# Optimization experiments

Hardware: AMD Instinct MI355X
Metric: run time of the kernel (lower is better)

The kernel has to match this reference:

```python
import jax, jax.numpy as jnp
import numpy as np

THRESH = 0.3
EPS = 1e-8
M = 256
D = 768


def setup_inputs() -> dict:
    key = jax.random.key(0)
    kx, kb, ka, kn = jax.random.split(key, 4)
    x = jax.random.normal(kx, (1, D), dtype=jnp.float32)
    base = jax.random.normal(kb, (M, D), dtype=jnp.float32)
    # correlate memories with x so that a realistic fraction passes the 0.3 cosine threshold
    alpha = jax.random.uniform(ka, (M,), minval=0.0, maxval=0.8)
    mem = alpha[:, None] * x[0][None, :] + jnp.sqrt(1.0 - alpha**2)[:, None] * base
    # pre-sampled injection noise (original: torch.randn * 0.1 per W element)
    noise = 0.1 * jax.random.normal(kn, (M, M, D), dtype=jnp.float32)
    return {"x": x, "mem": mem, "noise": noise}


def reference(x, mem, noise):
    # x: [1, D] query embedding; mem: [M, D] memory bank (k == memory embeddings)
    d = x.shape[-1]
    xv = x[0]                                   # [D]
    nx = jnp.maximum(jnp.linalg.norm(xv), EPS)
    nm = jnp.linalg.norm(mem, axis=-1)          # [M]
    nm_s = jnp.maximum(nm, EPS)
    Sx = xv.sum()
    Sm = mem.sum(-1)                            # [M]

    kx_dot = mem @ xv                           # [M] dot(k_i, x)
    mx_cos = kx_dot / (nm_s * nx)               # [M] cos(x, m_j) == cos(k_i, x)
    mask = (mx_cos > THRESH).astype(x.dtype)    # active memories A
    cnt = mask.sum()

    km_dot = mem @ mem.T                        # [M, M] dot(k_i, m_j)
    km_cos = km_dot / (nm_s[:, None] * nm_s[None, :])

    # c[a, i] = cos(k_i, m_a) + cos(k_i, x)  (scalar added to all D dims of k_i)
    c = km_cos.T + mx_cos[None, :]              # [M, M]

    # ||k'_{a,i}||^2 = ||k_i||^2 + 2 c sum(k_i) + D c^2
    nkp = jnp.sqrt(jnp.maximum(nm[None, :]**2 + 2.0 * c * Sm[None, :] + d * c**2, EPS**2))

    # cos(k'_{a,i}, x) = (dot(k_i,x) + c*sum(x)) / (||k'|| * ||x||)
    cos_kp_x = (kx_dot[None, :] + c * Sx) / (nkp * nx)

    # mean over a' in A of cos(k'_{a,i}, m_{a'}) in closed form
    A1 = (km_dot * (mask / nm_s)[None, :]).sum(-1)   # [M] (i-indexed)
    A2 = ((mask * Sm) / nm_s).sum()                  # scalar
    denom = nkp * jnp.maximum(cnt, 1.0)
    mean_cos_km = jnp.where(cnt > 0, (A1[None, :] + c * A2) / denom, 0.0)

    # W_{a,i} = k'_{a,i} + mean sim to x + mean sim to active mems; then noise; O_prev = 0
    W = mem[None, :, :] + (c + cos_kp_x + mean_cos_km)[:, :, None]   # [M, M, D]
    out = (W + noise) * mask[:, None, None]     # zero rows for inactive memories
    return out
```

## Files before the change

### kernel.cpp

```cpp
#include <hip/hip_runtime.h>
#include <hip/hip_bf16.h>
#include <math.h>

#define M 256
#define D 768
#define D4 (D/4)
#define THRESH 0.3
#define EPS 1e-8

typedef float vfloat4 __attribute__((ext_vector_type(4)));

#define WS_SM    0
#define WS_NM2   256
#define WS_KX    512
#define WS_MASK  768
#define WS_SX    1024
#define WS_NX2   1025
#define WS_MEMT  2048
#define WS_ST    (2048 + D * M)

__global__ __launch_bounds__(256) void k1_stats_transpose(const float* __restrict__ x,
                                                          const float* __restrict__ mem,
                                                          float* __restrict__ ws) {
    const int r = blockIdx.x;
    const int t = threadIdx.x;
    const float* row = (r < M) ? (mem + (size_t)r * D) : x;

    double s = 0.0, sq = 0.0, dt = 0.0;
    for (int d = t; d < D; d += 256) {
        float mf = row[d];
        double m = (double)mf;
        double xv = (double)x[d];
        s += m; sq += m * m; dt += m * xv;
        if (r < M) ws[WS_MEMT + (d >> 2) * (M * 4) + r * 4 + (d & 3)] = mf;
    }
    __shared__ double sh0[256], sh1[256], sh2[256];
    sh0[t] = s; sh1[t] = sq; sh2[t] = dt;
    __syncthreads();
    for (int k = 128; k > 0; k >>= 1) {
        if (t < k) { sh0[t] += sh0[t + k]; sh1[t] += sh1[t + k]; sh2[t] += sh2[t + k]; }
        __syncthreads();
    }
    if (t == 0) {
        if (r < M) {
            ws[WS_SM + r]  = (float)sh0[0];
            ws[WS_NM2 + r] = (float)sh1[0];
            ws[WS_KX + r]  = (float)sh2[0];
        } else {
            ws[WS_SX]  = (float)sh0[0];
            ws[WS_NX2] = (float)sh1[0];
        }
    }
}

__global__ __launch_bounds__(256) void k3_s(const float* __restrict__ mem,
                                            float* __restrict__ ws) {
    const int i = blockIdx.x;
    const int a = threadIdx.x;

    const double nx   = fmax(sqrt(fmax((double)ws[WS_NX2], 0.0)), EPS);
    const double Sx   = (double)ws[WS_SX];
    const double Sm_a = (double)ws[WS_SM + a];
    const double nm2a = (double)ws[WS_NM2 + a];
    const double kx_a = (double)ws[WS_KX + a];
    const double nmsa = fmax(sqrt(fmax(nm2a, 0.0)), EPS);
    const double mx_a = kx_a / (nmsa * nx);
    const double maska = (mx_a > THRESH) ? 1.0 : 0.0;
    const double w_a = maska / nmsa;
    ws[WS_MASK + a] = (float)maska;

    __shared__ vfloat4 lrow4[D4];
    if (a < D4) lrow4[a] = ((const vfloat4*)mem)[(size_t)i * D4 + a];
    __syncthreads();

    const vfloat4* memT4 = (const vfloat4*)(ws + WS_MEMT);
    float acc0 = 0.f, acc1 = 0.f, acc2 = 0.f, acc3 = 0.f;
    for (int dq = 0; dq < D4; dq += 4) {
        vfloat4 v0 = memT4[(dq + 0) * M + a]; vfloat4 l0 = lrow4[dq + 0];
        vfloat4 v1 = memT4[(dq + 1) * M + a]; vfloat4 l1 = lrow4[dq + 1];
        vfloat4 v2 = memT4[(dq + 2) * M + a]; vfloat4 l2 = lrow4[dq + 2];
        vfloat4 v3 = memT4[(dq + 3) * M + a]; vfloat4 l3 = lrow4[dq + 3];
        acc0 += v0.x * l0.x + v0.y * l0.y + v0.z * l0.z + v0.w * l0.w;
        acc1 += v1.x * l1.x + v1.y * l1.y + v1.z * l1.z + v1.w * l1.w;
        acc2 += v2.x * l2.x + v2.y * l2.y + v2.z * l2.z + v2.w * l2.w;
        acc3 += v3.x * l3.x + v3.y * l3.y + v3.z * l3.z + v3.w * l3.w;
    }
    const double g = (double)((acc0 + acc1) + (acc2 + acc3));

    __shared__ double shc[256], sha[256], shr[256];
    shc[a] = maska;
    sha[a] = maska * Sm_a / nmsa;
    shr[a] = w_a * g;
    __syncthreads();
    for (int k = 128; k > 0; k >>= 1) {
        if (a < k) { shc[a] += shc[a + k]; sha[a] += sha[a + k]; shr[a] += shr[a + k]; }
        __syncthreads();
    }
    const double cnt = shc[0];
    const double A2  = sha[0];
    const double A1  = shr[0];

    const double nm2i = (double)ws[WS_NM2 + i];
    const double Smi  = (double)ws[WS_SM + i];
    const double kxi  = (double)ws[WS_KX + i];
    const double nmsi = fmax(sqrt(fmax(nm2i, 0.0)), EPS);
    const double mxi  = kxi / (nmsi * nx);

    const double c = g / (nmsa * nmsi) + mxi;
    const double nkp = sqrt(fmax(nm2i + 2.0 * c * Smi + (double)D * c * c, EPS * EPS));
    const double cos_kp_x = (kxi + c * Sx) / (nkp * nx);
    const double mean_cos_km = (cnt > 0.0) ? (A1 + c * A2) / (nkp * fmax(cnt, 1.0)) : 0.0;

    ws[WS_ST + i * M + a] = (float)(c + cos_kp_x + mean_cos_km);
}

__global__ __launch_bounds__(D4) void k4_final(const float* __restrict__ mem,
                                               const float* __restrict__ noise,
                                               const float* __restrict__ ws,
                                               float* __restrict__ out) {
    const int a  = blockIdx.y;
    const int i0 = blockIdx.x * 32;
    const int t  = threadIdx.x;

    const vfloat4* mem4   = (const vfloat4*)mem;
    const vfloat4* noise4 = (const vfloat4*)noise;
    vfloat4* out4         = (vfloat4*)out;
    const size_t base = ((size_t)a * M + i0) * D4 + t;

    if (ws[WS_MASK + a] != 0.0f) {
        __shared__ float ssh[32];
        if (t < 32) ssh[t] = ws[WS_ST + (i0 + t) * M + a];
        __syncthreads();
        #pragma unroll 4
        for (int il = 0; il < 32; ++il) {
            const float s = ssh[il];
            vfloat4 m = mem4[(size_t)(i0 + il) * D4 + t];
            vfloat4 n = __builtin_nontemporal_load(noise4 + base + (size_t)il * D4);
            vfloat4 o;
            o.x = m.x + s + n.x;
            o.y = m.y + s + n.y;
            o.z = m.z + s + n.z;
            o.w = m.w + s + n.w;
            __builtin_nontemporal_store(o, out4 + base + (size_t)il * D4);
        }
    } else {
        const vfloat4 z = (vfloat4){0.f, 0.f, 0.f, 0.f};
        #pragma unroll 8
        for (int il = 0; il < 32; ++il)
            __builtin_nontemporal_store(z, out4 + base + (size_t)il * D4);
    }
}

extern "C" void kernel_launch(void* const* d_in, const int* in_sizes, int n_in,
                              void* d_out, int out_size, void* d_ws, size_t ws_size,
                              hipStream_t stream) {
    const float* x     = (const float*)d_in[0];
    const float* mem   = (const float*)d_in[1];
    const float* noise = (const float*)d_in[2];
    float* out = (float*)d_out;
    float* ws  = (float*)d_ws;

    k1_stats_transpose<<<dim3(M + 1), dim3(256), 0, stream>>>(x, mem, ws);
    k3_s<<<dim3(M), dim3(256), 0, stream>>>(mem, ws);
    k4_final<<<dim3(8, M), dim3(D4), 0, stream>>>(mem, noise, ws, out);
}
```

Measured before the change: 345.8 us.

## Move zero-row stores into k3, use fp32 math, and halve k4 tile

The zero-filling of output rows for inactive memories moves out of the final kernel into k3_s, so those stores overlap with the small Gram-matrix computation. k4_final now exits early for inactive rows. Its per-block row count drops from 32 to 16, doubling the grid. Most of k3's scalar math switches from double to float to cut FP64 cost, at some risk to precision near the threshold and in the reductions.

New measurement: 335.5 us. 3.0% less time.

```diff
diff --git a/kernel.cpp b/kernel.cpp
--- a/kernel.cpp
+++ b/kernel.cpp
@@ -54,24 +54,33 @@
 }
 
 __global__ __launch_bounds__(256) void k3_s(const float* __restrict__ mem,
-                                            float* __restrict__ ws) {
+                                            float* __restrict__ ws,
+                                            float* __restrict__ out) {
     const int i = blockIdx.x;
     const int a = threadIdx.x;
 
-    const double nx   = fmax(sqrt(fmax((double)ws[WS_NX2], 0.0)), EPS);
-    const double Sx   = (double)ws[WS_SX];
-    const double Sm_a = (double)ws[WS_SM + a];
-    const double nm2a = (double)ws[WS_NM2 + a];
-    const double kx_a = (double)ws[WS_KX + a];
-    const double nmsa = fmax(sqrt(fmax(nm2a, 0.0)), EPS);
-    const double mx_a = kx_a / (nmsa * nx);
-    const double maska = (mx_a > THRESH) ? 1.0 : 0.0;
-    const double w_a = maska / nmsa;
-    ws[WS_MASK + a] = (float)maska;
+    const double nxd   = fmax(sqrt(fmax((double)ws[WS_NX2], 0.0)), EPS);
+    const double nm2ad = (double)ws[WS_NM2 + a];
+    const double nmsad = fmax(sqrt(fmax(nm2ad, 0.0)), EPS);
+    const double mxad  = (double)ws[WS_KX + a] / (nmsad * nxd);
+    const float maska = (mxad > THRESH) ? 1.0f : 0.0f;
+    const float nmsa  = (float)nmsad;
+    if (i == 0) ws[WS_MASK + a] = maska;
 
+    __shared__ float shmask[M];
     __shared__ vfloat4 lrow4[D4];
+    shmask[a] = maska;
     if (a < D4) lrow4[a] = ((const vfloat4*)mem)[(size_t)i * D4 + a];
     __syncthreads();
+
+    if (a < D4) {
+        vfloat4* out4 = (vfloat4*)out;
+        const vfloat4 z = (vfloat4){0.f, 0.f, 0.f, 0.f};
+        for (int ap = 0; ap < M; ++ap) {
+            if (shmask[ap] == 0.0f)
+                __builtin_nontemporal_store(z, out4 + ((size_t)ap * M + i) * D4 + a);
+        }
+    }
 
     const vfloat4* memT4 = (const vfloat4*)(ws + WS_MEMT);
     float acc0 = 0.f, acc1 = 0.f, acc2 = 0.f, acc3 = 0.f;
@@ -85,41 +94,44 @@
         acc2 += v2.x * l2.x + v2.y * l2.y + v2.z * l2.z + v2.w * l2.w;
         acc3 += v3.x * l3.x + v3.y * l3.y + v3.z * l3.z + v3.w * l3.w;
     }
-    const double g = (double)((acc0 + acc1) + (acc2 + acc3));
+    const float g = (acc0 + acc1) + (acc2 + acc3);
 
-    __shared__ double shc[256], sha[256], shr[256];
+    __shared__ float shc[M], sha[M], shr[M];
     shc[a] = maska;
-    sha[a] = maska * Sm_a / nmsa;
-    shr[a] = w_a * g;
+    sha[a] = maska * ws[WS_SM + a] / nmsa;
+    shr[a] = (maska / nmsa) * g;
     __syncthreads();
     for (int k = 128; k > 0; k >>= 1) {
         if (a < k) { shc[a] += shc[a + k]; sha[a] += sha[a + k]; shr[a] += shr[a + k]; }
         __syncthreads();
     }
-    const double cnt = shc[0];
-    const double A2  = sha[0];
-    const double A1  = shr[0];
+    const float cnt = shc[0];
+    const float A2  = sha[0];
+    const float A1  = shr[0];
 
-    const double nm2i = (double)ws[WS_NM2 + i];
-    const double Smi  = (double)ws[WS_SM + i];
-    const double kxi  = (double)ws[WS_KX + i];
-    const double nmsi = fmax(sqrt(fmax(nm2i, 0.0)), EPS);
-    const double mxi  = kxi / (nmsi * nx);
+    const float nm2i = ws[WS_NM2 + i];
+    const float Smi  = ws[WS_SM + i];
+    const float kxi  = ws[WS_KX + i];
+    const float nmsi = fmaxf(sqrtf(fmaxf(nm2i, 0.f)), 1e-8f);
+    const float nx   = (float)nxd;
+    const float Sx   = ws[WS_SX];
+    const float mxi  = kxi / (nmsi * nx);
 
-    const double c = g / (nmsa * nmsi) + mxi;
-    const double nkp = sqrt(fmax(nm2i + 2.0 * c * Smi + (double)D * c * c, EPS * EPS));
-    const double cos_kp_x = (kxi + c * Sx) / (nkp * nx);
-    const double mean_cos_km = (cnt > 0.0) ? (A1 + c * A2) / (nkp * fmax(cnt, 1.0)) : 0.0;
+    const float c = g / (nmsa * nmsi) + mxi;
+    const float nkp = sqrtf(fmaxf(nm2i + 2.f * c * Smi + (float)D * c * c, 1e-16f));
+    const float cos_kp_x = (kxi + c * Sx) / (nkp * nx);
+    const float mean_cos_km = (cnt > 0.f) ? (A1 + c * A2) / (nkp * fmaxf(cnt, 1.f)) : 0.f;
 
-    ws[WS_ST + i * M + a] = (float)(c + cos_kp_x + mean_cos_km);
+    ws[WS_ST + i * M + a] = c + cos_kp_x + mean_cos_km;
 }
 
 __global__ __launch_bounds__(D4) void k4_final(const float* __restrict__ mem,
                                                const float* __restrict__ noise,
                                                const float* __restrict__ ws,
                                                float* __restrict__ out) {
-    const int a  = blockIdx.y;
-    const int i0 = blockIdx.x * 32;
+    const int a = blockIdx.y;
+    if (ws[WS_MASK + a] == 0.0f) return;
+    const int i0 = blockIdx.x * 16;
     const int t  = threadIdx.x;
 
     const vfloat4* mem4   = (const vfloat4*)mem;
@@ -127,27 +139,21 @@
     vfloat4* out4         = (vfloat4*)out;
     const size_t base = ((size_t)a * M + i0) * D4 + t;
 
-    if (ws[WS_MASK + a] != 0.0f) {
-        __shared__ float ssh[32];
-        if (t < 32) ssh[t] = ws[WS_ST + (i0 + t) * M + a];
-        __syncthreads();
-        #pragma unroll 4
-        for (int il = 0; il < 32; ++il) {
-            const float s = ssh[il];
-            vfloat4 m = mem4[(size_t)(i0 + il) * D4 + t];
-            vfloat4 n = __builtin_nontemporal_load(noise4 + base + (size_t)il * D4);
-            vfloat4 o;
-            o.x = m.x + s + n.x;
-            o.y = m.y + s + n.y;
-            o.z = m.z + s + n.z;
-            o.w = m.w + s + n.w;
-            __builtin_nontemporal_store(o, out4 + base + (size_t)il * D4);
-        }
-    } else {
-        const vfloat4 z = (vfloat4){0.f, 0.f, 0.f, 0.f};
-        #pragma unroll 8
-        for (int il = 0; il < 32; ++il)
-            __builtin_nontemporal_store(z, out4 + base + (size_t)il * D4);
+    __shared__ float ssh[16];
+    if (t < 16) ssh[t] = ws[WS_ST + (i0 + t) * M + a];
+    __syncthreads();
+
+    #pragma unroll 4
+    for (int il = 0; il < 16; ++il) {
+        const float s = ssh[il];
+        vfloat4 m = mem4[(size_t)(i0 + il) * D4 + t];
+        vfloat4 n = __builtin_nontemporal_load(noise4 + base + (size_t)il * D4);
+        vfloat4 o;
+        o.x = m.x + s + n.x;
+        o.y = m.y + s + n.y;
+        o.z = m.z + s + n.z;
+        o.w = m.w + s + n.w;
+        __builtin_nontemporal_store(o, out4 + base + (size_t)il * D4);
     }
 }
 
@@ -161,6 +167,6 @@
     float* ws  = (float*)d_ws;
 
     k1_stats_transpose<<<dim3(M + 1), dim3(256), 0, stream>>>(x, mem, ws);
-    k3_s<<<dim3(M), dim3(256), 0, stream>>>(mem, ws);
-    k4_final<<<dim3(8, M), dim3(D4), 0, stream>>>(mem, noise, ws, out);
+    k3_s<<<dim3(M), dim3(256), 0, stream>>>(mem, ws, out);
+    k4_final<<<dim3(16, M), dim3(D4), 0, stream>>>(mem, noise, ws, out);
 }
```
